# Performance work log

Measured on AMD Instinct MI355X. Metric: run time of the kernel, lower is better.

The kernel has to match this reference:

```python
import jax, jax.numpy as jnp
import numpy as np
from functools import partial

V, D, H, FF, NL, NC = 32000, 768, 12, 3072, 6, 1
B, L = 8, 512
EPS = 1e-5


def _layer_norm(x, g, b):
    m = jnp.mean(x, axis=-1, keepdims=True)
    v = jnp.mean((x - m) ** 2, axis=-1, keepdims=True)
    return (x - m) * jax.lax.rsqrt(v + EPS) * g + b


def setup_inputs() -> dict:
    key = jax.random.key(0)
    ks = jax.random.split(key, 24)
    s = 0.02
    inp = {
        'x': jax.random.randint(ks[0], (B, L), 0, V),
        'mask': jnp.ones((B, L), dtype=jnp.int32),
        'emb': jax.random.normal(ks[1], (V, D), jnp.float32) * s,
        # per-layer stacked params, leading dim = NL (scanned over)
        'Wq': jax.random.normal(ks[2], (NL, D, D), jnp.float32) * s,
        'bq': jnp.zeros((NL, D), jnp.float32),
        'Wk': jax.random.normal(ks[3], (NL, D, D), jnp.float32) * s,
        'bk': jnp.zeros((NL, D), jnp.float32),
        'Wv': jax.random.normal(ks[4], (NL, D, D), jnp.float32) * s,
        'bv': jnp.zeros((NL, D), jnp.float32),
        'Wo': jax.random.normal(ks[5], (NL, D, D), jnp.float32) * s,
        'bo': jnp.zeros((NL, D), jnp.float32),
        'W1': jax.random.normal(ks[6], (NL, D, FF), jnp.float32) * s,
        'b1': jnp.zeros((NL, FF), jnp.float32),
        'W2': jax.random.normal(ks[7], (NL, FF, D), jnp.float32) * s,
        'b2': jnp.zeros((NL, D), jnp.float32),
        'g1': jnp.ones((NL, D), jnp.float32),
        'be1': jnp.zeros((NL, D), jnp.float32),
        'g2': jnp.ones((NL, D), jnp.float32),
        'be2': jnp.zeros((NL, D), jnp.float32),
        'Wc': jax.random.normal(ks[8], (D, NC), jnp.float32) * s,
        'bc': jnp.zeros((NC,), jnp.float32),
    }
    return inp


def _forward(x, mask, emb, Wq, bq, Wk, bk, Wv, bv, Wo, bo, W1, b1, W2, b2,
             g1, be1, g2, be2, Wc, bc):
    Bx, Lx = x.shape
    Dm = emb.shape[1]
    dh = Dm // H
    scale = jnp.float32(np.sqrt(Dm / H))

    h = emb[x]  # [B,L,D]

    # PositionalEncoding (faithful to original buggy broadcast: pe[:B,0,:] added per-batch)
    pos = jnp.arange(Bx, dtype=jnp.float32)[:, None]
    div = jnp.exp(jnp.arange(0, Dm, 2, dtype=jnp.float32) * (-np.log(10000.0) / Dm))
    pe = jnp.stack([jnp.sin(pos * div), jnp.cos(pos * div)], axis=-1).reshape(Bx, Dm)
    h = h + pe[:, None, :]

    t = jnp.arange(Lx, dtype=jnp.float32)
    bias = -0.01 * (t[:, None] - t[None, :])  # [L,L]
    mask_b = (mask == 0)[:, None, None, :]    # [B,1,1,L]

    def step(h, p):
        (wq, bq_, wk, bk_, wv, bv_, wo, bo_, w1, b1_, w2, b2_,
         g1_, be1_, g2_, be2_) = p
        xn = _layer_norm(h, g1_, be1_)
        Q = (xn @ wq + bq_).reshape(Bx, Lx, H, dh)
        K = (xn @ wk + bk_).reshape(Bx, Lx, H, dh)
        Vv = (xn @ wv + bv_).reshape(Bx, Lx, H, dh)
        scores = jnp.einsum('bqhd,bkhd->bhqk', Q, K) / scale + bias
        scores = jnp.where(mask_b, -jnp.inf, scores)
        attn = jax.nn.softmax(scores, axis=-1)  # [B,H,L,L]
        out = jnp.einsum('bhqk,bkhd->bqhd', attn, Vv).reshape(Bx, Lx, Dm)
        h = h + (out @ wo + bo_)
        xn2 = _layer_norm(h, g2_, be2_)
        ff = jax.nn.gelu(xn2 @ w1 + b1_, approximate=False) @ w2 + b2_
        h = h + ff
        return h, attn

    params = (Wq, bq, Wk, bk, Wv, bv, Wo, bo, W1, b1, W2, b2, g1, be1, g2, be2)
    h, attn_all = jax.lax.scan(step, h, params)  # attn_all: [NL,B,H,L,L]
    logits = h[:, 0, :] @ Wc + bc  # CLS token -> [B,NC]
    return logits, attn_all


def reference(x, mask, emb, Wq, bq, Wk, bk, Wv, bv, Wo, bo, W1, b1, W2, b2,
              g1, be1, g2, be2, Wc, bc):
    return _forward(x, mask, emb, Wq, bq, Wk, bk, Wv, bv, Wo, bo,
                    W1, b1, W2, b2, g1, be1, g2, be2, Wc, bc)
```

## Files before the change

kernel.cpp:

```cpp
#include <hip/hip_runtime.h>
#include <math.h>

#define DMODEL 768
#define SEQL   512
#define NBATCH 8
#define NHEAD  12
#define NLAYER 6
#define FFDIM  3072
#define DHEAD  64
#define ROWS   (NBATCH * SEQL)
#define ATTN_PER_LAYER ((size_t)NBATCH * NHEAD * SEQL * SEQL)

using f32x4 = __attribute__((ext_vector_type(4))) float;
using f16x8 = __attribute__((ext_vector_type(8))) _Float16;
using f16x4 = __attribute__((ext_vector_type(4))) _Float16;

__device__ __forceinline__ void gload16(const void* g, void* l) {
    __builtin_amdgcn_global_load_lds(
        (const __attribute__((address_space(1))) unsigned int*)g,
        (__attribute__((address_space(3))) unsigned int*)l, 16, 0, 0);
}

__global__ __launch_bounds__(256) void embed_kernel(const int* __restrict__ x,
                                                    const float* __restrict__ emb,
                                                    float* __restrict__ h) {
    int bl = blockIdx.x;
    int b = bl >> 9;
    int tok = x[bl];
    const float* e = emb + (size_t)tok * DMODEL;
    float* hp = h + (size_t)bl * DMODEL;
    const float c = -0.011992632f;
#pragma unroll
    for (int u = 0; u < 3; ++u) {
        int d = threadIdx.x + u * 256;
        int i = d >> 1;
        float div = expf((float)(2 * i) * c);
        float ang = (float)b * div;
        float pe = (d & 1) ? cosf(ang) : sinf(ang);
        hp[d] = e[d] + pe;
    }
}

__global__ __launch_bounds__(256) void ln_kernel(const float* __restrict__ X,
                                                 const float* __restrict__ g,
                                                 const float* __restrict__ be,
                                                 _Float16* __restrict__ Yh,
                                                 _Float16* __restrict__ Yl) {
    int row = blockIdx.x;
    const float* x = X + (size_t)row * DMODEL;
    size_t base = (size_t)row * DMODEL;
    int t = threadIdx.x;
    float v0 = x[t], v1 = x[t + 256], v2 = x[t + 512];
    float s = v0 + v1 + v2;
    __shared__ float sb[8];
    for (int off = 32; off; off >>= 1) s += __shfl_down(s, off, 64);
    int lane = t & 63, wid = t >> 6;
    if (!lane) sb[wid] = s;
    __syncthreads();
    float mean = (sb[0] + sb[1] + sb[2] + sb[3]) * (1.0f / DMODEL);
    float d0 = v0 - mean, d1 = v1 - mean, d2 = v2 - mean;
    float q = d0 * d0 + d1 * d1 + d2 * d2;
    for (int off = 32; off; off >>= 1) q += __shfl_down(q, off, 64);
    if (!lane) sb[4 + wid] = q;
    __syncthreads();
    float var = (sb[4] + sb[5] + sb[6] + sb[7]) * (1.0f / DMODEL);
    float inv = 1.0f / sqrtf(var + 1e-5f);
    float y0 = d0 * inv * g[t] + be[t];
    float y1 = d1 * inv * g[t + 256] + be[t + 256];
    float y2 = d2 * inv * g[t + 512] + be[t + 512];
    _Float16 h0 = (_Float16)y0, h1 = (_Float16)y1, h2 = (_Float16)y2;
    Yh[base + t] = h0;       Yl[base + t] = (_Float16)(y0 - (float)h0);
    Yh[base + t + 256] = h1; Yl[base + t + 256] = (_Float16)(y1 - (float)h1);
    Yh[base + t + 512] = h2; Yl[base + t + 512] = (_Float16)(y2 - (float)h2);
}

__global__ __launch_bounds__(256) void wconv_kernel(const float* __restrict__ W,
                                                    _Float16* __restrict__ Th,
                                                    _Float16* __restrict__ Tl,
                                                    int K, int N) {
    __shared__ float t[32][33];
    int n0 = blockIdx.x * 32, k0 = blockIdx.y * 32;
    int tx = threadIdx.x & 31, ty = threadIdx.x >> 5;
#pragma unroll
    for (int u = 0; u < 4; ++u)
        t[ty + u * 8][tx] = W[(size_t)(k0 + ty + u * 8) * N + n0 + tx];
    __syncthreads();
#pragma unroll
    for (int u = 0; u < 4; ++u) {
        int r = ty + u * 8;
        float v = t[tx][r];
        _Float16 hi = (_Float16)v;
        size_t o = (size_t)(n0 + r) * K + k0 + tx;
        Th[o] = hi;
        Tl[o] = (_Float16)(v - (float)hi);
    }
}

__global__ __launch_bounds__(256) void bcat_kernel(const float* __restrict__ a,
                                                   const float* __restrict__ b,
                                                   const float* __restrict__ c,
                                                   float* __restrict__ o) {
    int t = blockIdx.x * 256 + threadIdx.x;
    o[t] = (t < DMODEL) ? a[t] : (t < 2 * DMODEL ? b[t - DMODEL] : c[t - 2 * DMODEL]);
}

__global__ __launch_bounds__(256) void vtrans_kernel(const _Float16* __restrict__ Vh,
                                                     const _Float16* __restrict__ Vl,
                                                     _Float16* __restrict__ Oh,
                                                     _Float16* __restrict__ Ol) {
    int kt = blockIdx.x, bh = blockIdx.y;
    int b = bh / NHEAD, hh = bh % NHEAD;
    int k0 = kt * 64;
    __shared__ _Float16 th[64][68];
    __shared__ _Float16 tl[64][68];
    int t = threadIdx.x;
    int r = t >> 2, c0 = (t & 3) * 16;
    size_t src = (size_t)(b * SEQL + k0 + r) * 2304 + 1536 + hh * DHEAD + c0;
#pragma unroll
    for (int u = 0; u < 4; ++u) {
        *(f16x4*)&th[r][c0 + u * 4] = *(const f16x4*)(Vh + src + u * 4);
        *(f16x4*)&tl[r][c0 + u * 4] = *(const f16x4*)(Vl + src + u * 4);
    }
    __syncthreads();
    int d = t >> 2, q4 = t & 3;
    size_t dst = ((size_t)bh * 64 + d) * SEQL + k0;
#pragma unroll
    for (int u = 0; u < 4; ++u) {
        int klo = (q4 + u * 4) * 4;
        f16x4 a, bb;
#pragma unroll
        for (int j = 0; j < 4; ++j) { a[j] = th[klo + j][d]; bb[j] = tl[klo + j][d]; }
        *(f16x4*)(Oh + dst + klo) = a;
        *(f16x4*)(Ol + dst + klo) = bb;
    }
}

__global__ __launch_bounds__(256) void attn_kernel(const _Float16* __restrict__ QKh,
                                                   const _Float16* __restrict__ QKl,
                                                   const int* __restrict__ mask,
                                                   float* __restrict__ P) {
    int qt = blockIdx.x, bh = blockIdx.y;
    int b = bh / NHEAD, hh = bh % NHEAD;
    int w = threadIdx.x >> 6, lane = threadIdx.x & 63;
    int fr = lane & 15, kg = lane >> 4;
    int q0 = qt * 64 + w * 16;

    __shared__ int msk[SEQL];
    msk[threadIdx.x] = mask[b * SEQL + threadIdx.x];
    msk[threadIdx.x + 256] = mask[b * SEQL + threadIdx.x + 256];
    __syncthreads();

    const _Float16* qrh = QKh + (size_t)(b * SEQL + q0 + fr) * 2304 + hh * DHEAD;
    const _Float16* qrl = QKl + (size_t)(b * SEQL + q0 + fr) * 2304 + hh * DHEAD;
    f16x8 ah0 = *(const f16x8*)(qrh + kg * 8);
    f16x8 ah1 = *(const f16x8*)(qrh + 32 + kg * 8);
    f16x8 al0 = *(const f16x8*)(qrl + kg * 8);
    f16x8 al1 = *(const f16x8*)(qrl + 32 + kg * 8);

    f32x4 acc[32];
#pragma unroll
    for (int nt = 0; nt < 32; ++nt)
#pragma unroll
        for (int r = 0; r < 4; ++r) acc[nt][r] = 0.0f;

    const _Float16* kbh = QKh + (size_t)(b * SEQL) * 2304 + DMODEL + hh * DHEAD;
    const _Float16* kbl = QKl + (size_t)(b * SEQL) * 2304 + DMODEL + hh * DHEAD;
#pragma unroll
    for (int nt = 0; nt < 32; ++nt) {
        const _Float16* krh = kbh + (size_t)(nt * 16 + fr) * 2304;
        const _Float16* krl = kbl + (size_t)(nt * 16 + fr) * 2304;
        f16x8 bh0 = *(const f16x8*)(krh + kg * 8);
        f16x8 bh1 = *(const f16x8*)(krh + 32 + kg * 8);
        f16x8 bl0 = *(const f16x8*)(krl + kg * 8);
        f16x8 bl1 = *(const f16x8*)(krl + 32 + kg * 8);
        f32x4 a = acc[nt];
        a = __builtin_amdgcn_mfma_f32_16x16x32_f16(ah0, bh0, a, 0, 0, 0);
        a = __builtin_amdgcn_mfma_f32_16x16x32_f16(ah1, bh1, a, 0, 0, 0);
        a = __builtin_amdgcn_mfma_f32_16x16x32_f16(ah0, bl0, a, 0, 0, 0);
        a = __builtin_amdgcn_mfma_f32_16x16x32_f16(ah1, bl1, a, 0, 0, 0);
        a = __builtin_amdgcn_mfma_f32_16x16x32_f16(al0, bh0, a, 0, 0, 0);
        a = __builtin_amdgcn_mfma_f32_16x16x32_f16(al1, bh1, a, 0, 0, 0);
        acc[nt] = a;
    }

    float mx[4] = {-INFINITY, -INFINITY, -INFINITY, -INFINITY};
#pragma unroll
    for (int nt = 0; nt < 32; ++nt) {
        int k = nt * 16 + fr;
        float bk = 0.01f * (float)k;
        bool dead = (msk[k] == 0);
#pragma unroll
        for (int r = 0; r < 4; ++r) {
            float s = acc[nt][r] * 0.125f - 0.01f * (float)(q0 + kg * 4 + r) + bk;
            if (dead) s = -INFINITY;
            acc[nt][r] = s;
            mx[r] = fmaxf(mx[r], s);
        }
    }
    float sm[4];
#pragma unroll
    for (int r = 0; r < 4; ++r) {
        float m = mx[r];
        m = fmaxf(m, __shfl_xor(m, 1, 64));
        m = fmaxf(m, __shfl_xor(m, 2, 64));
        m = fmaxf(m, __shfl_xor(m, 4, 64));
        m = fmaxf(m, __shfl_xor(m, 8, 64));
        mx[r] = m;
        sm[r] = 0.0f;
    }
#pragma unroll
    for (int nt = 0; nt < 32; ++nt)
#pragma unroll
        for (int r = 0; r < 4; ++r) {
            float e = expf(acc[nt][r] - mx[r]);
            acc[nt][r] = e;
            sm[r] += e;
        }
#pragma unroll
    for (int r = 0; r < 4; ++r) {
        float s = sm[r];
        s += __shfl_xor(s, 1, 64);
        s += __shfl_xor(s, 2, 64);
        s += __shfl_xor(s, 4, 64);
        s += __shfl_xor(s, 8, 64);
        sm[r] = 1.0f / s;
    }
    float* prow = P + ((size_t)bh * SEQL + q0 + kg * 4) * SEQL + fr;
#pragma unroll
    for (int r = 0; r < 4; ++r)
#pragma unroll
        for (int nt = 0; nt < 32; ++nt)
            prow[(size_t)r * SEQL + nt * 16] = acc[nt][r] * sm[r];
}

__global__ __launch_bounds__(256) void pv_kernel(const float* __restrict__ P,
                                                 const _Float16* __restrict__ Vth,
                                                 const _Float16* __restrict__ Vtl,
                                                 _Float16* __restrict__ Oh,
                                                 _Float16* __restrict__ Ol) {
    int qt = blockIdx.x, bh = blockIdx.y;
    int b = bh / NHEAD, hh = bh % NHEAD;
    int w = threadIdx.x >> 6, lane = threadIdx.x & 63;
    int fr = lane & 15, kg = lane >> 4;
    int q0 = qt * 64 + w * 16;

    const float* prow = P + ((size_t)bh * SEQL + q0 + fr) * SEQL + kg * 8;
    const _Float16* vbh[4];
    const _Float16* vbl[4];
#pragma unroll
    for (int nf = 0; nf < 4; ++nf) {
        size_t o = ((size_t)bh * 64 + nf * 16 + fr) * SEQL + kg * 8;
        vbh[nf] = Vth + o;
        vbl[nf] = Vtl + o;
    }
    f32x4 acc[4];
#pragma unroll
    for (int nf = 0; nf < 4; ++nf)
#pragma unroll
        for (int r = 0; r < 4; ++r) acc[nf][r] = 0.0f;

#pragma unroll
    for (int ks = 0; ks < 16; ++ks) {
        float4 p0 = *(const float4*)(prow + ks * 32);
        float4 p1 = *(const float4*)(prow + ks * 32 + 4);
        float pv[8] = {p0.x, p0.y, p0.z, p0.w, p1.x, p1.y, p1.z, p1.w};
        f16x8 ph, pl;
#pragma unroll
        for (int e = 0; e < 8; ++e) {
            _Float16 hv = (_Float16)pv[e];
            ph[e] = hv;
            pl[e] = (_Float16)(pv[e] - (float)hv);
        }
#pragma unroll
        for (int nf = 0; nf < 4; ++nf) {
            f16x8 vh = *(const f16x8*)(vbh[nf] + ks * 32);
            f16x8 vl = *(const f16x8*)(vbl[nf] + ks * 32);
            acc[nf] = __builtin_amdgcn_mfma_f32_16x16x32_f16(ph, vh, acc[nf], 0, 0, 0);
            acc[nf] = __builtin_amdgcn_mfma_f32_16x16x32_f16(ph, vl, acc[nf], 0, 0, 0);
            acc[nf] = __builtin_amdgcn_mfma_f32_16x16x32_f16(pl, vh, acc[nf], 0, 0, 0);
        }
    }
#pragma unroll
    for (int nf = 0; nf < 4; ++nf)
#pragma unroll
        for (int r = 0; r < 4; ++r) {
            size_t o = (size_t)(b * SEQL + q0 + kg * 4 + r) * DMODEL + hh * DHEAD + nf * 16 + fr;
            float v = acc[nf][r];
            _Float16 hv = (_Float16)v;
            Oh[o] = hv;
            Ol[o] = (_Float16)(v - (float)hv);
        }
}

__global__ __launch_bounds__(256) void mgemm_kernel(
    const _Float16* __restrict__ Ah, const _Float16* __restrict__ Al,
    const _Float16* __restrict__ Bh, const _Float16* __restrict__ Bl,
    const float* __restrict__ bias, float* __restrict__ C,
    _Float16* __restrict__ Ch, _Float16* __restrict__ Cl,
    int N, int K, int flags) {
    __shared__ __attribute__((aligned(16))) _Float16 Ash[128][32];
    __shared__ __attribute__((aligned(16))) _Float16 Asl[128][32];
    __shared__ __attribute__((aligned(16))) _Float16 Bsh[128][32];
    __shared__ __attribute__((aligned(16))) _Float16 Bsl[128][32];

    int tid = threadIdx.x;
    int w = tid >> 6, lane = tid & 63;
    int m0 = blockIdx.y * 128, n0 = blockIdx.x * 128;
    int kper = K / gridDim.z;
    int kbeg = blockIdx.z * kper;

    int srow = lane >> 2;
    int kch = (lane & 3) ^ ((lane >> 3) & 3);
    size_t aoff0 = (size_t)(m0 + w * 16 + srow) * K + kch * 8;
    size_t aoff1 = (size_t)(m0 + (w + 4) * 16 + srow) * K + kch * 8;
    size_t boff0 = (size_t)(n0 + w * 16 + srow) * K + kch * 8;
    size_t boff1 = (size_t)(n0 + (w + 4) * 16 + srow) * K + kch * 8;
    _Float16* lAh0 = &Ash[w * 16][0];
    _Float16* lAh1 = &Ash[(w + 4) * 16][0];
    _Float16* lAl0 = &Asl[w * 16][0];
    _Float16* lAl1 = &Asl[(w + 4) * 16][0];
    _Float16* lBh0 = &Bsh[w * 16][0];
    _Float16* lBh1 = &Bsh[(w + 4) * 16][0];
    _Float16* lBl0 = &Bsl[w * 16][0];
    _Float16* lBl1 = &Bsl[(w + 4) * 16][0];

    int fr = lane & 15, kg = lane >> 4;
    int kb = (kg ^ ((fr >> 1) & 3)) * 8;
    int wr = w >> 1, wc = w & 1;

    f32x4 acc[4][4];
#pragma unroll
    for (int i = 0; i < 4; ++i)
#pragma unroll
        for (int j = 0; j < 4; ++j)
#pragma unroll
            for (int r = 0; r < 4; ++r) acc[i][j][r] = 0.0f;

    for (int k0 = kbeg; k0 < kbeg + kper; k0 += 32) {
        gload16(Ah + aoff0 + k0, lAh0);
        gload16(Ah + aoff1 + k0, lAh1);
        gload16(Al + aoff0 + k0, lAl0);
        gload16(Al + aoff1 + k0, lAl1);
        gload16(Bh + boff0 + k0, lBh0);
        gload16(Bh + boff1 + k0, lBh1);
        gload16(Bl + boff0 + k0, lBl0);
        gload16(Bl + boff1 + k0, lBl1);
        asm volatile("s_waitcnt vmcnt(0)" ::: "memory");
        __syncthreads();

        f16x8 a_h[4], a_l[4], b_h[4], b_l[4];
#pragma unroll
        for (int i = 0; i < 4; ++i) {
            int r = wr * 64 + i * 16 + fr;
            a_h[i] = *(const f16x8*)&Ash[r][kb];
            a_l[i] = *(const f16x8*)&Asl[r][kb];
        }
#pragma unroll
        for (int j = 0; j < 4; ++j) {
            int r = wc * 64 + j * 16 + fr;
            b_h[j] = *(const f16x8*)&Bsh[r][kb];
            b_l[j] = *(const f16x8*)&Bsl[r][kb];
        }
#pragma unroll
        for (int i = 0; i < 4; ++i)
#pragma unroll
            for (int j = 0; j < 4; ++j) {
                acc[i][j] = __builtin_amdgcn_mfma_f32_16x16x32_f16(a_h[i], b_h[j], acc[i][j], 0, 0, 0);
                acc[i][j] = __builtin_amdgcn_mfma_f32_16x16x32_f16(a_h[i], b_l[j], acc[i][j], 0, 0, 0);
                acc[i][j] = __builtin_amdgcn_mfma_f32_16x16x32_f16(a_l[i], b_h[j], acc[i][j], 0, 0, 0);
            }
        __syncthreads();
    }

    int od = kg * 4;
#pragma unroll
    for (int j = 0; j < 4; ++j) {
        int col = n0 + wc * 64 + j * 16 + fr;
        float bv = (bias && blockIdx.z == 0) ? bias[col] : 0.0f;
#pragma unroll
        for (int i = 0; i < 4; ++i) {
#pragma unroll
            for (int r = 0; r < 4; ++r) {
                int rowg = m0 + wr * 64 + i * 16 + od + r;
                float v = acc[i][j][r] + bv;
                if (flags & 1) v = 0.5f * v * (1.0f + erff(v * 0.70710678118654752f));
                size_t o = (size_t)rowg * N + col;
                if (flags & 4) {
                    _Float16 hv = (_Float16)v;
                    Ch[o] = hv;
                    Cl[o] = (_Float16)(v - (float)hv);
                } else if (flags & 2) {
                    unsafeAtomicAdd(&C[o], v);
                } else {
                    C[o] = v;
                }
            }
        }
    }
}

__global__ __launch_bounds__(256) void logits_kernel(const float* __restrict__ h,
                                                     const float* __restrict__ Wc,
                                                     const float* __restrict__ bc,
                                                     float* __restrict__ out) {
    int b = blockIdx.x;
    const float* hp = h + (size_t)b * SEQL * DMODEL;
    int t = threadIdx.x;
    float s = hp[t] * Wc[t] + hp[t + 256] * Wc[t + 256] + hp[t + 512] * Wc[t + 512];
    __shared__ float sb[4];
    for (int off = 32; off; off >>= 1) s += __shfl_down(s, off, 64);
    int lane = t & 63, wid = t >> 6;
    if (!lane) sb[wid] = s;
    __syncthreads();
    if (t == 0) out[b] = sb[0] + sb[1] + sb[2] + sb[3] + bc[0];
}

extern "C" void kernel_launch(void* const* d_in, const int* in_sizes, int n_in,
                              void* d_out, int out_size, void* d_ws, size_t ws_size,
                              hipStream_t stream) {
    (void)in_sizes; (void)n_in; (void)out_size; (void)ws_size;
    const int*   x    = (const int*)d_in[0];
    const int*   mask = (const int*)d_in[1];
    const float* emb  = (const float*)d_in[2];
    const float* Wq   = (const float*)d_in[3];
    const float* bq   = (const float*)d_in[4];
    const float* Wk   = (const float*)d_in[5];
    const float* bk   = (const float*)d_in[6];
    const float* Wv   = (const float*)d_in[7];
    const float* bv   = (const float*)d_in[8];
    const float* Wo   = (const float*)d_in[9];
    const float* bo   = (const float*)d_in[10];
    const float* W1   = (const float*)d_in[11];
    const float* b1   = (const float*)d_in[12];
    const float* W2   = (const float*)d_in[13];
    const float* b2   = (const float*)d_in[14];
    const float* g1   = (const float*)d_in[15];
    const float* be1  = (const float*)d_in[16];
    const float* g2   = (const float*)d_in[17];
    const float* be2  = (const float*)d_in[18];
    const float* Wc   = (const float*)d_in[19];
    const float* bc   = (const float*)d_in[20];

    float* out  = (float*)d_out;
    float* attn = out + NBATCH * 1;

    const size_t RD  = (size_t)ROWS * DMODEL;
    const size_t RFF = (size_t)ROWS * FFDIM;
    const size_t DD  = (size_t)DMODEL * DMODEL;
    const size_t DF  = (size_t)DMODEL * FFDIM;

    float* ws   = (float*)d_ws;
    float* h    = ws;
    _Float16* xnh  = (_Float16*)(h + RD);
    _Float16* xnl  = xnh + RD;
    _Float16* qkvh = xnl + RD;
    _Float16* qkvl = qkvh + 3 * RD;
    _Float16* vth  = qkvl + 3 * RD;
    _Float16* vtl  = vth + RD;
    _Float16* atth = vtl + RD;
    _Float16* attl = atth + RD;
    _Float16* ffh  = attl + RD;
    _Float16* ffl  = ffh + RFF;
    _Float16* wqkvh = ffl + RFF;
    _Float16* wqkvl = wqkvh + 3 * DD;
    _Float16* woh  = wqkvl + 3 * DD;
    _Float16* wol  = woh + DD;
    _Float16* w1h  = wol + DD;
    _Float16* w1l  = w1h + DF;
    _Float16* w2h  = w1l + DF;
    _Float16* w2l  = w2h + DF;
    float* bqkv = (float*)(w2l + DF);

    embed_kernel<<<ROWS, 256, 0, stream>>>(x, emb, h);

    for (int l = 0; l < NLAYER; ++l) {
        const float* wq = Wq + (size_t)l * DD;
        const float* wk = Wk + (size_t)l * DD;
        const float* wv = Wv + (size_t)l * DD;
        const float* wo = Wo + (size_t)l * DD;
        const float* w1 = W1 + (size_t)l * DF;
        const float* w2 = W2 + (size_t)l * DF;
        float* P = attn + (size_t)l * ATTN_PER_LAYER;

        wconv_kernel<<<dim3(24, 24), 256, 0, stream>>>(wq, wqkvh,          wqkvl,          DMODEL, DMODEL);
        wconv_kernel<<<dim3(24, 24), 256, 0, stream>>>(wk, wqkvh + DD,     wqkvl + DD,     DMODEL, DMODEL);
        wconv_kernel<<<dim3(24, 24), 256, 0, stream>>>(wv, wqkvh + 2 * DD, wqkvl + 2 * DD, DMODEL, DMODEL);
        wconv_kernel<<<dim3(24, 24), 256, 0, stream>>>(wo, woh, wol, DMODEL, DMODEL);
        wconv_kernel<<<dim3(96, 24), 256, 0, stream>>>(w1, w1h, w1l, DMODEL, FFDIM);
        wconv_kernel<<<dim3(24, 96), 256, 0, stream>>>(w2, w2h, w2l, FFDIM, DMODEL);
        bcat_kernel<<<9, 256, 0, stream>>>(bq + l * DMODEL, bk + l * DMODEL, bv + l * DMODEL, bqkv);

        ln_kernel<<<ROWS, 256, 0, stream>>>(h, g1 + l * DMODEL, be1 + l * DMODEL, xnh, xnl);

        mgemm_kernel<<<dim3(18, 32, 1), 256, 0, stream>>>(
            xnh, xnl, wqkvh, wqkvl, bqkv, nullptr, qkvh, qkvl,
            3 * DMODEL, DMODEL, 4);

        vtrans_kernel<<<dim3(SEQL / 64, NBATCH * NHEAD), 256, 0, stream>>>(
            qkvh, qkvl, vth, vtl);

        attn_kernel<<<dim3(SEQL / 64, NBATCH * NHEAD), 256, 0, stream>>>(
            qkvh, qkvl, mask, P);

        pv_kernel<<<dim3(SEQL / 64, NBATCH * NHEAD), 256, 0, stream>>>(
            P, vth, vtl, atth, attl);

        mgemm_kernel<<<dim3(6, 32, 2), 256, 0, stream>>>(
            atth, attl, woh, wol, bo + l * DMODEL, h, nullptr, nullptr,
            DMODEL, DMODEL, 2);

        ln_kernel<<<ROWS, 256, 0, stream>>>(h, g2 + l * DMODEL, be2 + l * DMODEL, xnh, xnl);

        mgemm_kernel<<<dim3(24, 32, 1), 256, 0, stream>>>(
            xnh, xnl, w1h, w1l, b1 + l * FFDIM, nullptr, ffh, ffl,
            FFDIM, DMODEL, 1 | 4);

        mgemm_kernel<<<dim3(6, 32, 4), 256, 0, stream>>>(
            ffh, ffl, w2h, w2l, b2 + l * DMODEL, h, nullptr, nullptr,
            DMODEL, FFDIM, 2);
    }

    logits_kernel<<<NBATCH, 256, 0, stream>>>(h, Wc, bc, out);
}
```

Before: 3.681 ms.

## Double-buffer LDS tiles in split-fp16 GEMM to overlap loads with MFMA

The mgemm kernel now keeps two LDS buffers per operand and issues the global-to-LDS loads for the next K tile before computing on the current one. This replaces the two __syncthreads per iteration with one barrier, so load latency can overlap the MFMA work. In exchange the kernel uses twice the shared memory (64KB), which can lower occupancy. Whether a single barrier per iteration fully protects the buffer being overwritten from late readers is unclear.

```diff
diff --git a/kernel.cpp b/kernel.cpp
--- a/kernel.cpp
+++ b/kernel.cpp
@@ -298,10 +298,10 @@
     const float* __restrict__ bias, float* __restrict__ C,
     _Float16* __restrict__ Ch, _Float16* __restrict__ Cl,
     int N, int K, int flags) {
-    __shared__ __attribute__((aligned(16))) _Float16 Ash[128][32];
-    __shared__ __attribute__((aligned(16))) _Float16 Asl[128][32];
-    __shared__ __attribute__((aligned(16))) _Float16 Bsh[128][32];
-    __shared__ __attribute__((aligned(16))) _Float16 Bsl[128][32];
+    __shared__ __attribute__((aligned(16))) _Float16 Ash[2][128][32];
+    __shared__ __attribute__((aligned(16))) _Float16 Asl[2][128][32];
+    __shared__ __attribute__((aligned(16))) _Float16 Bsh[2][128][32];
+    __shared__ __attribute__((aligned(16))) _Float16 Bsl[2][128][32];
 
     int tid = threadIdx.x;
     int w = tid >> 6, lane = tid & 63;
@@ -315,14 +315,7 @@
     size_t aoff1 = (size_t)(m0 + (w + 4) * 16 + srow) * K + kch * 8;
     size_t boff0 = (size_t)(n0 + w * 16 + srow) * K + kch * 8;
     size_t boff1 = (size_t)(n0 + (w + 4) * 16 + srow) * K + kch * 8;
-    _Float16* lAh0 = &Ash[w * 16][0];
-    _Float16* lAh1 = &Ash[(w + 4) * 16][0];
-    _Float16* lAl0 = &Asl[w * 16][0];
-    _Float16* lAl1 = &Asl[(w + 4) * 16][0];
-    _Float16* lBh0 = &Bsh[w * 16][0];
-    _Float16* lBh1 = &Bsh[(w + 4) * 16][0];
-    _Float16* lBl0 = &Bsl[w * 16][0];
-    _Float16* lBl1 = &Bsl[(w + 4) * 16][0];
+    int r0 = w * 16, r1 = (w + 4) * 16;
 
     int fr = lane & 15, kg = lane >> 4;
     int kb = (kg ^ ((fr >> 1) & 3)) * 8;
@@ -336,30 +329,50 @@
 #pragma unroll
             for (int r = 0; r < 4; ++r) acc[i][j][r] = 0.0f;
 
-    for (int k0 = kbeg; k0 < kbeg + kper; k0 += 32) {
-        gload16(Ah + aoff0 + k0, lAh0);
-        gload16(Ah + aoff1 + k0, lAh1);
-        gload16(Al + aoff0 + k0, lAl0);
-        gload16(Al + aoff1 + k0, lAl1);
-        gload16(Bh + boff0 + k0, lBh0);
-        gload16(Bh + boff1 + k0, lBh1);
-        gload16(Bl + boff0 + k0, lBl0);
-        gload16(Bl + boff1 + k0, lBl1);
+    int nt = kper >> 5;
+    {
+        int k0 = kbeg;
+        gload16(Ah + aoff0 + k0, &Ash[0][r0][0]);
+        gload16(Ah + aoff1 + k0, &Ash[0][r1][0]);
+        gload16(Al + aoff0 + k0, &Asl[0][r0][0]);
+        gload16(Al + aoff1 + k0, &Asl[0][r1][0]);
+        gload16(Bh + boff0 + k0, &Bsh[0][r0][0]);
+        gload16(Bh + boff1 + k0, &Bsh[0][r1][0]);
+        gload16(Bl + boff0 + k0, &Bsl[0][r0][0]);
+        gload16(Bl + boff1 + k0, &Bsl[0][r1][0]);
+    }
+
+    for (int t = 0; t < nt; ++t) {
+        int cur = t & 1;
         asm volatile("s_waitcnt vmcnt(0)" ::: "memory");
-        __syncthreads();
+        __builtin_amdgcn_s_barrier();
+        __builtin_amdgcn_sched_barrier(0);
+
+        if (t + 1 < nt) {
+            int k0 = kbeg + (t + 1) * 32;
+            int nb = cur ^ 1;
+            gload16(Ah + aoff0 + k0, &Ash[nb][r0][0]);
+            gload16(Ah + aoff1 + k0, &Ash[nb][r1][0]);
+            gload16(Al + aoff0 + k0, &Asl[nb][r0][0]);
+            gload16(Al + aoff1 + k0, &Asl[nb][r1][0]);
+            gload16(Bh + boff0 + k0, &Bsh[nb][r0][0]);
+            gload16(Bh + boff1 + k0, &Bsh[nb][r1][0]);
+            gload16(Bl + boff0 + k0, &Bsl[nb][r0][0]);
+            gload16(Bl + boff1 + k0, &Bsl[nb][r1][0]);
+        }
 
         f16x8 a_h[4], a_l[4], b_h[4], b_l[4];
 #pragma unroll
         for (int i = 0; i < 4; ++i) {
             int r = wr * 64 + i * 16 + fr;
-            a_h[i] = *(const f16x8*)&Ash[r][kb];
-            a_l[i] = *(const f16x8*)&Asl[r][kb];
+            a_h[i] = *(const f16x8*)&Ash[cur][r][kb];
+            a_l[i] = *(const f16x8*)&Asl[cur][r][kb];
         }
 #pragma unroll
         for (int j = 0; j < 4; ++j) {
             int r = wc * 64 + j * 16 + fr;
-            b_h[j] = *(const f16x8*)&Bsh[r][kb];
-            b_l[j] = *(const f16x8*)&Bsl[r][kb];
+            b_h[j] = *(const f16x8*)&Bsh[cur][r][kb];
+            b_l[j] = *(const f16x8*)&Bsl[cur][r][kb];
         }
 #pragma unroll
         for (int i = 0; i < 4; ++i)
@@ -369,7 +382,6 @@
                 acc[i][j] = __builtin_amdgcn_mfma_f32_16x16x32_f16(a_h[i], b_l[j], acc[i][j], 0, 0, 0);
                 acc[i][j] = __builtin_amdgcn_mfma_f32_16x16x32_f16(a_l[i], b_h[j], acc[i][j], 0, 0, 0);
             }
-        __syncthreads();
     }
 
     int od = kg * 4;
```

Result: faster. 3.600 ms (-2.2%).
